# Performance work log

Measured on AMD Instinct MI355X. Metric: run time of the kernel, lower is better.

The kernel has to match this reference:

```python
import jax, jax.numpy as jnp
import numpy as np

PARA_CH = 256
FEATURE_CH = 256
PI = 3.14159  # matches the literal in the torch source


def _linear_params(key, fan_in, fan_out):
    kw, kb = jax.random.split(key)
    bound = 1.0 / np.sqrt(fan_in)
    W = jax.random.uniform(kw, (fan_in, fan_out), minval=-bound, maxval=bound, dtype=jnp.float32)
    b = jax.random.uniform(kb, (fan_out,), minval=-bound, maxval=bound, dtype=jnp.float32)
    return W, b


def setup_inputs() -> dict:
    key = jax.random.key(0)
    ks = jax.random.split(key, 6)
    feature_map = jax.random.normal(ks[0], (4, FEATURE_CH, 128, 128), dtype=jnp.float32)
    para_code = jax.random.normal(ks[1], (4, PARA_CH), dtype=jnp.float32)
    W1, b1 = _linear_params(ks[2], PARA_CH, PARA_CH)
    Ws, bs = _linear_params(ks[3], PARA_CH, FEATURE_CH)
    Wr, br = _linear_params(ks[4], PARA_CH, FEATURE_CH)
    Wt, bt = _linear_params(ks[5], PARA_CH, 2 * FEATURE_CH)
    return {"feature_map": feature_map, "para_code": para_code,
            "W1": W1, "b1": b1, "Ws": Ws, "bs": bs,
            "Wr": Wr, "br": br, "Wt": Wt, "bt": bt}


def _coord_1d(n):
    # align_corners=True-style normalized coordinates, as in make_coordinate_grid_3d
    return 2.0 * (jnp.arange(n, dtype=jnp.float32) / (n - 1)) - 1.0


def _trilinear_sample_zeros(vol, gx, gy, gz):
    """F.grid_sample 5D equivalent: mode='bilinear' (trilinear), padding_mode='zeros',
    align_corners=False. vol: [B,D,H,W] (channel dim of size 1 squeezed out);
    gx,gy,gz: [B,Do,Ho,Wo] normalized coords. Returns [B,Do,Ho,Wo]."""
    B, D, H, W = vol.shape
    ix = ((gx + 1.0) * W - 1.0) * 0.5
    iy = ((gy + 1.0) * H - 1.0) * 0.5
    iz = ((gz + 1.0) * D - 1.0) * 0.5
    x0f, y0f, z0f = jnp.floor(ix), jnp.floor(iy), jnp.floor(iz)
    wx, wy, wz = ix - x0f, iy - y0f, iz - z0f
    x0 = x0f.astype(jnp.int32); x1 = x0 + 1
    y0 = y0f.astype(jnp.int32); y1 = y0 + 1
    z0 = z0f.astype(jnp.int32); z1 = z0 + 1
    vflat = vol.reshape(B, -1)

    def gather(zi, yi, xi):
        valid = (zi >= 0) & (zi < D) & (yi >= 0) & (yi < H) & (xi >= 0) & (xi < W)
        zc = jnp.clip(zi, 0, D - 1)
        yc = jnp.clip(yi, 0, H - 1)
        xc = jnp.clip(xi, 0, W - 1)
        flat = (zc * H + yc) * W + xc  # [B,Do,Ho,Wo]
        v = jnp.take_along_axis(vflat, flat.reshape(B, -1), axis=1).reshape(flat.shape)
        return jnp.where(valid, v, 0.0)

    out = (gather(z0, y0, x0) * (1 - wz) * (1 - wy) * (1 - wx)
           + gather(z0, y0, x1) * (1 - wz) * (1 - wy) * wx
           + gather(z0, y1, x0) * (1 - wz) * wy * (1 - wx)
           + gather(z0, y1, x1) * (1 - wz) * wy * wx
           + gather(z1, y0, x0) * wz * (1 - wy) * (1 - wx)
           + gather(z1, y0, x1) * wz * (1 - wy) * wx
           + gather(z1, y1, x0) * wz * wy * (1 - wx)
           + gather(z1, y1, x1) * wz * wy * wx)
    return out


def reference(feature_map, para_code, W1, b1, Ws, bs, Wr, br, Wt, bt):
    B, C, H, W = feature_map.shape  # C == feature_ch == depth of 3D grid
    p = jax.nn.relu(para_code @ W1 + b1)                      # [B, para_ch]
    scale = jax.nn.sigmoid(p @ Ws + bs) * 2.0                 # [B, C]
    angle = jnp.tanh(p @ Wr + br) * PI                        # [B, C]
    translation = jnp.tanh(p @ Wt + bt).reshape(B, C, 2)      # [B, C, 2]
    ca, sa = jnp.cos(angle), jnp.sin(angle)
    # rotation matrix [[cos, -sin], [sin, cos]] per (batch, channel)
    rot = jnp.stack([jnp.stack([ca, -sa], -1), jnp.stack([sa, ca], -1)], -2)  # [B,C,2,2]

    x = _coord_1d(W)  # [W]
    y = _coord_1d(H)  # [H]
    z = _coord_1d(C)  # [C] (depth == channel dim)
    grid_xy = jnp.stack(jnp.broadcast_arrays(x[None, None, :], y[None, :, None]), -1)  # [1,H,W,2] -> broadcast to [C,H,W,2]
    grid_xy = jnp.broadcast_to(grid_xy, (C, H, W, 2))

    # per-pixel affine transform: rot @ [x,y] * scale + trans
    trans_grid = jnp.einsum('bcij,chwj->bchwi', rot, grid_xy)
    trans_grid = trans_grid * scale[:, :, None, None, None] + translation[:, :, None, None, :]
    gx = trans_grid[..., 0]
    gy = trans_grid[..., 1]
    gz = jnp.broadcast_to(z[None, :, None, None], (B, C, H, W))

    return _trilinear_sample_zeros(feature_map, gx, gy, gz)  # [B,C,H,W]
```

## Files before the change

### kernel.cpp

```cpp
#include <hip/hip_runtime.h>
#include <math.h>

#define BATCH 4
#define CH    256
#define HH    128
#define WW    128
#define PC    256
#define PI_F  3.14159f
#define PLANE (HH * WW)
#define NP    4

#define PSTRIDE 134
#define PROWS   131
#define BUFSZ   (PROWS * PSTRIDE)

__device__ __forceinline__ void barrier_lds() {
    asm volatile("s_waitcnt lgkmcnt(0)\n\ts_barrier" ::: "memory");
}

struct Stage { float4 a[4]; float4 b[4]; };

__device__ __forceinline__ Stage stage_load(const float* __restrict__ pl0,
                                            const float* __restrict__ pl1, int t) {
    Stage s;
#pragma unroll
    for (int j = 0; j < 4; ++j) {
        const int f = 4 * (t + 1024 * j);
        s.a[j] = *(const float4*)(pl0 + f);
        s.b[j] = *(const float4*)(pl1 + f);
    }
    return s;
}

__device__ __forceinline__ void stage_store_pad(float* __restrict__ buf, const Stage& s,
                                                float wz0, float wz1, int t) {
#pragma unroll
    for (int j = 0; j < 4; ++j) {
        const int f = 4 * (t + 1024 * j);
        const int y = f >> 7, x = f & (WW - 1);
        float* p = &buf[(y + 1) * PSTRIDE + (x + 1)];
        p[0] = fmaf(wz0, s.a[j].x, wz1 * s.b[j].x);
        p[1] = fmaf(wz0, s.a[j].y, wz1 * s.b[j].y);
        p[2] = fmaf(wz0, s.a[j].z, wz1 * s.b[j].z);
        p[3] = fmaf(wz0, s.a[j].w, wz1 * s.b[j].w);
    }
}

__device__ __forceinline__ void gather_plane(const float* __restrict__ buf,
                                             const float4 P,
                                             float* __restrict__ outp,
                                             const float yf, const int xi) {
    const float cA  = P.x, cB = P.y;
    float ixp = fmaf(cA, (float)xi, fmaf(-cB, yf, P.z));
    float iyp = fmaf(cB, (float)xi, fmaf( cA, yf, P.w));
    const float dx8 = 8.0f * cA, dy8 = 8.0f * cB;
#pragma unroll 4
    for (int k = 0; k < 16; ++k) {
        const float xc  = fminf(fmaxf(ixp, 0.0f), 129.99f);
        const float yc  = fminf(fmaxf(iyp, 0.0f), 129.99f);
        const float x0f = floorf(xc), y0f = floorf(yc);
        const float fx  = xc - x0f,   fy  = yc - y0f;
        const int   a   = (int)y0f * PSTRIDE + (int)x0f;
        const float v00 = buf[a],           v01 = buf[a + 1];
        const float v10 = buf[a + PSTRIDE], v11 = buf[a + PSTRIDE + 1];
        const float h0  = fmaf(fx, v01 - v00, v00);
        const float h1  = fmaf(fx, v11 - v10, v10);
        outp[k * 8 + xi] = fmaf(fy, h1 - h0, h0);
        ixp += dx8; iyp += dy8;
    }
}

__global__ __launch_bounds__(1024, 4)
void adaat_fused_kernel(const float* __restrict__ fm,
                        const float* __restrict__ pc,
                        const float* __restrict__ W1, const float* __restrict__ b1,
                        const float* __restrict__ Ws, const float* __restrict__ bs,
                        const float* __restrict__ Wr, const float* __restrict__ br,
                        const float* __restrict__ Wt, const float* __restrict__ bt,
                        float* __restrict__ out) {
    __shared__ float  lds[2 * BUFSZ];
    __shared__ float  red[1024];
    __shared__ float  p_sh[PC];
    __shared__ float  sh_head[16];
    __shared__ float4 sh_par[NP];

    const int t   = threadIdx.x;
    const int bc0 = blockIdx.x * NP;
    const int b   = bc0 >> 8;

    const float* base = fm + (size_t)b * (CH * PLANE);
    const float* pl0[NP]; const float* pl1[NP];
    float w0[NP], w1[NP];
#pragma unroll
    for (int i = 0; i < NP; ++i) {
        const int   c  = (bc0 + i) & (CH - 1);
        const float iz = (256.0f / 255.0f) * (float)c - 0.5f;
        const float zf = floorf(iz);
        const float fz = iz - zf;
        const int   z0 = (int)zf;
        w0[i]  = (z0 >= 0)     ? (1.0f - fz) : 0.0f;
        w1[i]  = (z0 + 1 < CH) ? fz          : 0.0f;
        pl0[i] = base + (size_t)max(z0, 0)          * PLANE;
        pl1[i] = base + (size_t)min(z0 + 1, CH - 1) * PLANE;
    }

    Stage s = stage_load(pl0[0], pl1[0], t);

#pragma unroll
    for (int i = 0; i < 35; ++i) {
        const int idx = t + 1024 * i;
        if (idx < 2 * BUFSZ) lds[idx] = 0.0f;
    }

    {
        const int jj = t & 255, kk = t >> 8;
        const float* pcb = pc + b * PC + kk * 64;
        const float* w   = W1 + (kk * 64) * PC + jj;
        float acc = 0.0f;
#pragma unroll 8
        for (int i = 0; i < 64; ++i)
            acc = fmaf(pcb[i], w[i * PC], acc);
        red[t] = acc;
    }
    barrier_lds();
    if (t < 256)
        p_sh[t] = fmaxf(red[t] + red[256 + t] + red[512 + t] + red[768 + t] + b1[t], 0.0f);
    barrier_lds();

    stage_store_pad(&lds[0], s, w0[0], w1[0], t);

    const int wv = t >> 6, l = t & 63;
    {
        const int q  = wv >> 2;
        const int h  = wv & 3;
        const int cq = (bc0 + q) & (CH - 1);
        const float* wp; int stride;
        if      (h == 0) { wp = Ws + cq;                stride = PC;     }
        else if (h == 1) { wp = Wr + cq;                stride = PC;     }
        else             { wp = Wt + 2 * cq + (h == 3); stride = 2 * PC; }
        float dot = 0.0f;
#pragma unroll
        for (int m = 0; m < 4; ++m) {
            const int k = l + 64 * m;
            dot = fmaf(p_sh[k], wp[(size_t)k * stride], dot);
        }
#pragma unroll
        for (int off = 32; off >= 1; off >>= 1)
            dot += __shfl_xor(dot, off, 64);
        if (l == 0) sh_head[wv] = dot;
    }
    barrier_lds();

    if (t < NP) {
        const int cq = (bc0 + t) & (CH - 1);
        const float s2  = 2.0f / (1.0f + expf(-(sh_head[4 * t] + bs[cq])));
        const float ang = tanhf(sh_head[4 * t + 1] + br[cq]) * PI_F;
        float sa, ca;
        sincosf(ang, &sa, &ca);
        const float A  = s2 * ca, B = s2 * sa;
        const float Tx = tanhf(sh_head[4 * t + 2] + bt[2 * cq]);
        const float Ty = tanhf(sh_head[4 * t + 3] + bt[2 * cq + 1]);
        sh_par[t] = make_float4(A * (128.0f / 127.0f),
                                B * (128.0f / 127.0f),
                                64.0f * (Tx - A + B) + 64.5f,
                                64.0f * (Ty - A - B) + 64.5f);
    }
    barrier_lds();

    const int   xi = l & 7;
    const int   yj = wv * 8 + (l >> 3);
    const float yf = (float)yj;

#pragma unroll
    for (int i = 1; i < NP; ++i) {
        s = stage_load(pl0[i], pl1[i], t);
        gather_plane(&lds[((i - 1) & 1) * BUFSZ], sh_par[i - 1],
                     out + (size_t)(bc0 + i - 1) * PLANE + yj * WW, yf, xi);
        stage_store_pad(&lds[(i & 1) * BUFSZ], s, w0[i], w1[i], t);
        barrier_lds();
    }
    gather_plane(&lds[((NP - 1) & 1) * BUFSZ], sh_par[NP - 1],
                 out + (size_t)(bc0 + NP - 1) * PLANE + yj * WW, yf, xi);
}

extern "C" void kernel_launch(void* const* d_in, const int* in_sizes, int n_in,
                              void* d_out, int out_size, void* d_ws, size_t ws_size,
                              hipStream_t stream) {
    const float* feature_map = (const float*)d_in[0];
    const float* para_code   = (const float*)d_in[1];
    const float* W1 = (const float*)d_in[2];
    const float* b1 = (const float*)d_in[3];
    const float* Ws = (const float*)d_in[4];
    const float* bs = (const float*)d_in[5];
    const float* Wr = (const float*)d_in[6];
    const float* br = (const float*)d_in[7];
    const float* Wt = (const float*)d_in[8];
    const float* bt = (const float*)d_in[9];

    adaat_fused_kernel<<<BATCH * CH / NP, 1024, 0, stream>>>(
        feature_map, para_code, W1, b1, Ws, bs, Wr, br, Wt, bt, (float*)d_out);
}
```

Baseline: 150.9 us.

## Prefetch two planes ahead and vectorize gather output stores as float4

The global-load pipeline now keeps two plane loads in flight, so the second plane is fetched during the MLP head computation and each later load is issued one stage earlier. The first plane's LDS store moves after the head computation. The gather loop now has each thread produce four consecutive x pixels and write them as one float4, instead of strided scalar stores. The deeper prefetch doubles the register footprint of staged data, which may hurt occupancy under the 1024-thread launch bounds.

```diff
diff --git a/kernel.cpp b/kernel.cpp
--- a/kernel.cpp
+++ b/kernel.cpp
@@ -50,23 +50,31 @@
                                              const float4 P,
                                              float* __restrict__ outp,
                                              const float yf, const int xi) {
-    const float cA  = P.x, cB = P.y;
-    float ixp = fmaf(cA, (float)xi, fmaf(-cB, yf, P.z));
-    float iyp = fmaf(cB, (float)xi, fmaf( cA, yf, P.w));
-    const float dx8 = 8.0f * cA, dy8 = 8.0f * cB;
-#pragma unroll 4
-    for (int k = 0; k < 16; ++k) {
-        const float xc  = fminf(fmaxf(ixp, 0.0f), 129.99f);
-        const float yc  = fminf(fmaxf(iyp, 0.0f), 129.99f);
-        const float x0f = floorf(xc), y0f = floorf(yc);
-        const float fx  = xc - x0f,   fy  = yc - y0f;
-        const int   a   = (int)y0f * PSTRIDE + (int)x0f;
-        const float v00 = buf[a],           v01 = buf[a + 1];
-        const float v10 = buf[a + PSTRIDE], v11 = buf[a + PSTRIDE + 1];
-        const float h0  = fmaf(fx, v01 - v00, v00);
-        const float h1  = fmaf(fx, v11 - v10, v10);
-        outp[k * 8 + xi] = fmaf(fy, h1 - h0, h0);
-        ixp += dx8; iyp += dy8;
+    const float cA = P.x, cB = P.y;
+    const float xb = (float)(xi * 4);
+    float ixp = fmaf(cA, xb, fmaf(-cB, yf, P.z));
+    float iyp = fmaf(cB, xb, fmaf( cA, yf, P.w));
+    const float dx32 = 32.0f * cA, dy32 = 32.0f * cB;
+#pragma unroll
+    for (int k = 0; k < 4; ++k) {
+        float4 r;
+        float ix = ixp, iy = iyp;
+#pragma unroll
+        for (int j = 0; j < 4; ++j) {
+            const float xc  = fminf(fmaxf(ix, 0.0f), 129.99f);
+            const float yc  = fminf(fmaxf(iy, 0.0f), 129.99f);
+            const float x0f = floorf(xc), y0f = floorf(yc);
+            const float fx  = xc - x0f,   fy  = yc - y0f;
+            const int   a   = (int)y0f * PSTRIDE + (int)x0f;
+            const float v00 = buf[a],           v01 = buf[a + 1];
+            const float v10 = buf[a + PSTRIDE], v11 = buf[a + PSTRIDE + 1];
+            const float h0  = fmaf(fx, v01 - v00, v00);
+            const float h1  = fmaf(fx, v11 - v10, v10);
+            (&r.x)[j] = fmaf(fy, h1 - h0, h0);
+            ix += cA; iy += cB;
+        }
+        *(float4*)(outp + k * 32 + xi * 4) = r;
+        ixp += dx32; iyp += dy32;
     }
 }
 
@@ -104,7 +112,8 @@
         pl1[i] = base + (size_t)min(z0 + 1, CH - 1) * PLANE;
     }
 
-    Stage s = stage_load(pl0[0], pl1[0], t);
+    Stage sA = stage_load(pl0[0], pl1[0], t);
+    Stage sB = stage_load(pl0[1], pl1[1], t);
 
 #pragma unroll
     for (int i = 0; i < 35; ++i) {
@@ -126,8 +135,6 @@
     if (t < 256)
         p_sh[t] = fmaxf(red[t] + red[256 + t] + red[512 + t] + red[768 + t] + b1[t], 0.0f);
     barrier_lds();
-
-    stage_store_pad(&lds[0], s, w0[0], w1[0], t);
 
     const int wv = t >> 6, l = t & 63;
     {
@@ -165,22 +172,30 @@
                                 64.0f * (Tx - A + B) + 64.5f,
                                 64.0f * (Ty - A - B) + 64.5f);
     }
+
+    stage_store_pad(&lds[0], sA, w0[0], w1[0], t);
     barrier_lds();
 
     const int   xi = l & 7;
     const int   yj = wv * 8 + (l >> 3);
     const float yf = (float)yj;
-
-#pragma unroll
-    for (int i = 1; i < NP; ++i) {
-        s = stage_load(pl0[i], pl1[i], t);
-        gather_plane(&lds[((i - 1) & 1) * BUFSZ], sh_par[i - 1],
-                     out + (size_t)(bc0 + i - 1) * PLANE + yj * WW, yf, xi);
-        stage_store_pad(&lds[(i & 1) * BUFSZ], s, w0[i], w1[i], t);
-        barrier_lds();
-    }
-    gather_plane(&lds[((NP - 1) & 1) * BUFSZ], sh_par[NP - 1],
-                 out + (size_t)(bc0 + NP - 1) * PLANE + yj * WW, yf, xi);
+    float* outb = out + (size_t)bc0 * PLANE + yj * WW;
+
+    sA = stage_load(pl0[2], pl1[2], t);
+    gather_plane(&lds[0], sh_par[0], outb, yf, xi);
+    stage_store_pad(&lds[BUFSZ], sB, w0[1], w1[1], t);
+    barrier_lds();
+
+    sB = stage_load(pl0[3], pl1[3], t);
+    gather_plane(&lds[BUFSZ], sh_par[1], outb + PLANE, yf, xi);
+    stage_store_pad(&lds[0], sA, w0[2], w1[2], t);
+    barrier_lds();
+
+    gather_plane(&lds[0], sh_par[2], outb + 2 * PLANE, yf, xi);
+    stage_store_pad(&lds[BUFSZ], sB, w0[3], w1[3], t);
+    barrier_lds();
+
+    gather_plane(&lds[BUFSZ], sh_par[3], outb + 3 * PLANE, yf, xi);
 }
 
 extern "C" void kernel_launch(void* const* d_in, const int* in_sizes, int n_in,
```

Result: no change. 152.7 us (+1.2%).
